# Performance work log

Hardware: AMD Instinct MI355X
Metric: run time of the kernel (lower is better)

## Reference

```python
import jax, jax.numpy as jnp
import numpy as np

D_MODEL = 1024
NUM_HEADS = 16
HEAD_DIM = D_MODEL // NUM_HEADS
SEQ_LEN = 2048
BATCH = 2
THETA = 10000.0


def apply_rope(x, token_positions):
    # x: (..., seq, head_dim); token_positions: (seq,)
    d_k = x.shape[-1]
    inv_freq = 1.0 / (THETA ** (jnp.arange(0, d_k, 2, dtype=jnp.float32) / d_k))  # (d_k/2,)
    angle = token_positions.astype(jnp.float32)[:, None] * inv_freq[None, :]       # (seq, d_k/2)
    cos, sin = jnp.cos(angle), jnp.sin(angle)
    xr = x.reshape(*x.shape[:-1], d_k // 2, 2)
    a, b = xr[..., 0], xr[..., 1]  # real, imag parts of consecutive pairs
    # complex multiply (a + ib) * (cos + i sin)
    out_r = a * cos - b * sin
    out_i = a * sin + b * cos
    return jnp.stack([out_r, out_i], axis=-1).reshape(x.shape)


def setup_inputs() -> dict:
    key = jax.random.key(0)
    ks = jax.random.split(key, 5)
    std = np.sqrt(2.0 / (D_MODEL + D_MODEL))
    return {
        "x": jax.random.normal(ks[0], (BATCH, SEQ_LEN, D_MODEL), dtype=jnp.float32),
        "Wq": jax.random.normal(ks[1], (D_MODEL, D_MODEL), dtype=jnp.float32) * std,
        "Wk": jax.random.normal(ks[2], (D_MODEL, D_MODEL), dtype=jnp.float32) * std,
        "Wv": jax.random.normal(ks[3], (D_MODEL, D_MODEL), dtype=jnp.float32) * std,
        "Wo": jax.random.normal(ks[4], (D_MODEL, D_MODEL), dtype=jnp.float32) * std,
        "token_positions": jnp.arange(SEQ_LEN, dtype=jnp.int32),
    }


def reference(x, Wq, Wk, Wv, Wo, token_positions):
    B, L, D = x.shape
    H, Dh = NUM_HEADS, HEAD_DIM

    def proj(W):  # '... d_in, d_out d_in -> ... d_out' then split heads -> (B,H,L,Dh)
        y = jnp.einsum('bld,ed->ble', x, W)
        return y.reshape(B, L, H, Dh).transpose(0, 2, 1, 3)

    q = apply_rope(proj(Wq), token_positions)
    k = apply_rope(proj(Wk), token_positions)
    v = proj(Wv)

    scores = jnp.einsum('bhqd,bhkd->bhqk', q, k) / jnp.sqrt(jnp.float32(Dh))  # (B,H,L,L)
    causal = jnp.tril(jnp.ones((L, L), dtype=bool))
    scores = jnp.where(causal, scores, -jnp.inf)
    attn = jax.nn.softmax(scores, axis=-1)
    o = jnp.einsum('bhqk,bhkd->bhqd', attn, v)  # (B,H,L,Dh)
    o = o.transpose(0, 2, 1, 3).reshape(B, L, D)
    return jnp.einsum('bld,ed->ble', o, Wo)
```

## Files before the change

kernel.cpp:

```cpp
#include <hip/hip_runtime.h>

typedef __bf16 bf16;
typedef __attribute__((ext_vector_type(8))) __bf16 bf16x8;
typedef __attribute__((ext_vector_type(4))) __bf16 bf16x4;
typedef __attribute__((ext_vector_type(4))) float f32x4;

__device__ inline bf16 f2bf(float f) {
  unsigned u = __builtin_bit_cast(unsigned, f);
  u += 0x7fff + ((u >> 16) & 1);
  unsigned short h = (unsigned short)(u >> 16);
  return __builtin_bit_cast(bf16, h);
}

__device__ inline void gl_lds16(const bf16* g, bf16* l) {
  __builtin_amdgcn_global_load_lds(
      (const __attribute__((address_space(1))) void*)g,
      (__attribute__((address_space(3))) void*)l, 16, 0, 0);
}

__global__ __launch_bounds__(256) void cvt_kernel(
    const float* __restrict__ x, const float* __restrict__ wq,
    const float* __restrict__ wk, const float* __restrict__ wv,
    const float* __restrict__ wo, bf16* __restrict__ dst,
    const int* __restrict__ pos, float* __restrict__ tab) {
  if (blockIdx.x >= 8192) {
    int gid = (blockIdx.x - 8192) * 256 + threadIdx.x;
    int tok = gid >> 5, j = gid & 31;
    float freq = exp2f(-(float)(2 * j) * 0.20762051f);
    float angle = (float)pos[tok] * freq;
    float sn, cs;
    sincosf(angle, &sn, &cs);
    *(float2*)(tab + tok * 64 + j * 2) = make_float2(cs, sn);
    return;
  }
  int idx = (blockIdx.x * 256 + threadIdx.x) * 4;
  const float* src;
  if (idx < 4194304) {
    src = x + idx;
  } else {
    int j = idx - 4194304;
    int w = j >> 20;
    const float* sw = (w == 0) ? wq : (w == 1) ? wk : (w == 2) ? wv : wo;
    src = sw + (j & 1048575);
  }
  float4 f = *(const float4*)src;
  bf16x4 o = {f2bf(f.x), f2bf(f.y), f2bf(f.z), f2bf(f.w)};
  *(bf16x4*)(dst + idx) = o;
}

__global__ __launch_bounds__(256) void gemm_qkv_kernel(
    const bf16* __restrict__ xb, const bf16* __restrict__ wb,
    const float* __restrict__ tab,
    bf16* __restrict__ Qb, bf16* __restrict__ Kb, bf16* __restrict__ Vtb) {
  __shared__ __align__(16) bf16 smem[16384];
  bf16* As = smem;
  bf16* Bs = smem + 8192;
  int tid = threadIdx.x;
  int lane = tid & 63, w = tid >> 6;
  int l15 = lane & 15, quad = lane >> 4;
  int bid = blockIdx.x;
  int xcd = bid & 7, j = bid >> 3;
  int by = (xcd & 3) * 8 + (j & 7);
  int bx = (xcd >> 2) * 12 + (j >> 3);
  int mb = by * 128, nb = bx * 128;
  int mq = (w & 1) * 64, nq = (w >> 1) * 64;
  int gsw = (lane & 7) ^ ((lane >> 3) & 7);
  const bf16* agp = xb + (size_t)(mb + w * 32 + (lane >> 3)) * 1024 + gsw * 8;
  const bf16* bgp = wb + (size_t)(nb + w * 32 + (lane >> 3)) * 1024 + gsw * 8;
  bf16* alp = As + (w * 32) * 64;
  bf16* blp = Bs + (w * 32) * 64;
  f32x4 acc[4][4];
#pragma unroll
  for (int i = 0; i < 4; ++i)
#pragma unroll
    for (int j2 = 0; j2 < 4; ++j2)
      for (int r = 0; r < 4; ++r) acc[i][j2][r] = 0.f;
  for (int kt = 0; kt < 16; ++kt) {
#pragma unroll
    for (int i = 0; i < 4; ++i) {
      gl_lds16(agp + i * 8192, alp + i * 512);
      gl_lds16(bgp + i * 8192, blp + i * 512);
    }
    agp += 64; bgp += 64;
    __syncthreads();
#pragma unroll
    for (int c = 0; c < 2; ++c) {
      bf16x8 af[4], bfr[4];
      int rg = (c * 4 + quad);
#pragma unroll
      for (int mt = 0; mt < 4; ++mt)
        af[mt] = *(const bf16x8*)(As + (mq + mt * 16 + l15) * 64 + (rg ^ (l15 & 7)) * 8);
#pragma unroll
      for (int nt = 0; nt < 4; ++nt)
        bfr[nt] = *(const bf16x8*)(Bs + (nq + nt * 16 + l15) * 64 + (rg ^ (l15 & 7)) * 8);
#pragma unroll
      for (int mt = 0; mt < 4; ++mt)
#pragma unroll
        for (int nt = 0; nt < 4; ++nt)
          acc[mt][nt] = __builtin_amdgcn_mfma_f32_16x16x32_bf16(af[mt], bfr[nt], acc[mt][nt], 0, 0, 0);
    }
    __syncthreads();
  }
  int b = mb >> 11;
  int mtok = mb & 2047;
  if (bx < 16) {
    bf16* dst = (bx < 8) ? Qb : Kb;
#pragma unroll
    for (int nt = 0; nt < 4; ++nt) {
      int e = nb + nq + nt * 16 + l15;
      int d = e & 63;
      int h = (e & 1023) >> 6;
      int tbase = d & ~1;
#pragma unroll
      for (int mt = 0; mt < 4; ++mt) {
#pragma unroll
        for (int r = 0; r < 4; ++r) {
          int ltok = mtok + mq + mt * 16 + quad * 4 + r;
          float val = acc[mt][nt][r];
          float p = __shfl_xor(val, 1);
          float2 cs2 = *(const float2*)(tab + ltok * 64 + tbase);
          float outv = (e & 1) ? (p * cs2.y + val * cs2.x) : (val * cs2.x - p * cs2.y);
          dst[(size_t)(((b << 4) + h) * 2048 + ltok) * 64 + d] = f2bf(outv);
        }
      }
    }
  } else {
    bf16* T = smem;
    for (int h2 = 0; h2 < 2; ++h2) {
      if ((w >> 1) == h2) {
#pragma unroll
        for (int nt = 0; nt < 4; ++nt)
#pragma unroll
          for (int mt = 0; mt < 4; ++mt) {
            bf16x4 tv = {f2bf(acc[mt][nt][0]), f2bf(acc[mt][nt][1]),
                         f2bf(acc[mt][nt][2]), f2bf(acc[mt][nt][3])};
            *(bf16x4*)&T[(nt * 16 + l15) * 136 + mq + mt * 16 + quad * 4] = tv;
          }
      }
      __syncthreads();
      int row = tid >> 2, cs = (tid & 3) * 32;
      int e = nb + h2 * 64 + row;
      int d = e & 63, hh = (e & 1023) >> 6;
      bf16* vdst = Vtb + ((size_t)((b << 4) + hh) * 64 + d) * 2048 + mtok + cs;
#pragma unroll
      for (int j3 = 0; j3 < 4; ++j3)
        *(bf16x8*)(vdst + j3 * 8) = *(const bf16x8*)&T[row * 136 + cs + j3 * 8];
      __syncthreads();
    }
  }
}

#define SCALE_L2E 0.18033688f
__global__ __launch_bounds__(256) void attn_kernel(
    const bf16* __restrict__ Qb, const bf16* __restrict__ Kb,
    const bf16* __restrict__ Vtb, bf16* __restrict__ Ob) {
  __shared__ __align__(16) bf16 Ks[64 * 64];
  __shared__ __align__(16) bf16 Vs[64 * 64];
  __shared__ __align__(16) bf16 pbuf[4][16 * 72];
  int tid = threadIdx.x;
  int lane = tid & 63, w = tid >> 6;
  int l15 = lane & 15, quad = lane >> 4;
  int bidx = blockIdx.x;
  int bh = bidx & 31;
  int qt = 31 - (bidx >> 5);
  int qbase = qt * 64;
  const bf16* Qp = Qb + (size_t)bh * 131072;
  const bf16* Kp = Kb + (size_t)bh * 131072;
  const bf16* Vp = Vtb + (size_t)bh * 131072;
  int r8 = lane >> 3;
  int gsw8 = (lane & 7) ^ r8;
  int g0 = quad ^ (l15 & 7);
  int g1 = (4 + quad) ^ (l15 & 7);
  bf16x8 qf[2];
#pragma unroll
  for (int c = 0; c < 2; ++c)
    qf[c] = *(const bf16x8*)(Qp + (size_t)(qbase + w * 16 + l15) * 64 + c * 32 + quad * 8);
  f32x4 oacc[4];
#pragma unroll
  for (int dt = 0; dt < 4; ++dt)
    for (int r = 0; r < 4; ++r) oacc[dt][r] = 0.f;
  float lpart = 0.f;
  int qmin_w = qbase + w * 16;
  int qmax_w = qmin_w + 15;
  int ntiles = qt + 1;

  for (int t = 0; t < ntiles; ++t) {
    int kb = t * 64;
    {
      const bf16* ksrc = Kp + (size_t)(kb + w * 16 + r8) * 64 + gsw8 * 8;
      bf16* kdst = &Ks[(w * 16) * 64];
      gl_lds16(ksrc, kdst);
      gl_lds16(ksrc + 8 * 64, kdst + 8 * 64);
      const bf16* vsrc = Vp + (size_t)(w * 16 + r8) * 2048 + kb + gsw8 * 8;
      bf16* vdst = &Vs[(w * 16) * 64];
      gl_lds16(vsrc, vdst);
      gl_lds16(vsrc + 8 * 2048, vdst + 8 * 64);
    }
    __syncthreads();
    if (kb <= qmax_w) {
      bf16x8 kf[4][2], vf[4][2];
#pragma unroll
      for (int kt = 0; kt < 4; ++kt) {
        kf[kt][0] = *(const bf16x8*)(&Ks[(kt * 16 + l15) * 64 + g0 * 8]);
        kf[kt][1] = *(const bf16x8*)(&Ks[(kt * 16 + l15) * 64 + g1 * 8]);
      }
#pragma unroll
      for (int dt = 0; dt < 4; ++dt) {
        vf[dt][0] = *(const bf16x8*)(&Vs[(dt * 16 + l15) * 64 + g0 * 8]);
        vf[dt][1] = *(const bf16x8*)(&Vs[(dt * 16 + l15) * 64 + g1 * 8]);
      }
      int q = qmin_w + l15;
      f32x4 s[4];
#pragma unroll
      for (int kt = 0; kt < 4; ++kt) {
        for (int r = 0; r < 4; ++r) s[kt][r] = 0.f;
        s[kt] = __builtin_amdgcn_mfma_f32_16x16x32_bf16(kf[kt][0], qf[0], s[kt], 0, 0, 0);
        s[kt] = __builtin_amdgcn_mfma_f32_16x16x32_bf16(kf[kt][1], qf[1], s[kt], 0, 0, 0);
      }
      float pe[16];
      if (kb + 63 > qmin_w) {
#pragma unroll
        for (int kt = 0; kt < 4; ++kt)
#pragma unroll
          for (int r = 0; r < 4; ++r) {
            int key = kb + kt * 16 + quad * 4 + r;
            pe[kt * 4 + r] = (key <= q) ? exp2f(s[kt][r] * SCALE_L2E) : 0.f;
          }
      } else {
#pragma unroll
        for (int kt = 0; kt < 4; ++kt)
#pragma unroll
          for (int r = 0; r < 4; ++r) pe[kt * 4 + r] = exp2f(s[kt][r] * SCALE_L2E);
      }
#pragma unroll
      for (int i = 0; i < 16; ++i) lpart += pe[i];
#pragma unroll
      for (int kt = 0; kt < 4; ++kt) {
        bf16x4 pw = {f2bf(pe[kt * 4]), f2bf(pe[kt * 4 + 1]), f2bf(pe[kt * 4 + 2]), f2bf(pe[kt * 4 + 3])};
        *(bf16x4*)&pbuf[w][l15 * 72 + kt * 16 + quad * 4] = pw;
      }
      bf16x8 pb0 = *(const bf16x8*)&pbuf[w][l15 * 72 + quad * 8];
      bf16x8 pb1 = *(const bf16x8*)&pbuf[w][l15 * 72 + 32 + quad * 8];
#pragma unroll
      for (int dt = 0; dt < 4; ++dt) {
        oacc[dt] = __builtin_amdgcn_mfma_f32_16x16x32_bf16(vf[dt][0], pb0, oacc[dt], 0, 0, 0);
        oacc[dt] = __builtin_amdgcn_mfma_f32_16x16x32_bf16(vf[dt][1], pb1, oacc[dt], 0, 0, 0);
      }
    }
    __syncthreads();
  }
  float lrun = lpart;
  lrun += __shfl_xor(lrun, 16);
  lrun += __shfl_xor(lrun, 32);
  int b0 = bh >> 4, h = bh & 15;
  float inv = 1.f / lrun;
  int q = qmin_w + l15;
  bf16* obase = Ob + ((size_t)(b0 * 2048 + q)) * 1024 + h * 64;
#pragma unroll
  for (int dt = 0; dt < 4; ++dt)
#pragma unroll
    for (int r = 0; r < 4; ++r)
      obase[dt * 16 + quad * 4 + r] = f2bf(oacc[dt][r] * inv);
}

__global__ __launch_bounds__(256) void gemm_out_kernel(
    const bf16* __restrict__ Ob, const bf16* __restrict__ wob,
    float* __restrict__ out) {
  __shared__ __align__(16) bf16 As[128 * 64];
  __shared__ __align__(16) bf16 Bs[64 * 64];
  int tid = threadIdx.x;
  int lane = tid & 63, w = tid >> 6;
  int l15 = lane & 15, quad = lane >> 4;
  int bid = blockIdx.x;
  int xcd = bid & 7, j = bid >> 3;
  int by = (xcd & 3) * 8 + (j & 7);
  int bx = (xcd >> 2) * 8 + (j >> 3);
  int mb = by * 128, nb = bx * 64;
  int mq = (w & 1) * 64, nq = (w >> 1) * 32;
  int gsw = (lane & 7) ^ ((lane >> 3) & 7);
  const bf16* agp = Ob + (size_t)(mb + w * 32 + (lane >> 3)) * 1024 + gsw * 8;
  const bf16* bgp = wob + (size_t)(nb + w * 16 + (lane >> 3)) * 1024 + gsw * 8;
  bf16* alp = As + (w * 32) * 64;
  bf16* blp = Bs + (w * 16) * 64;
  f32x4 acc[4][2];
#pragma unroll
  for (int i = 0; i < 4; ++i)
#pragma unroll
    for (int j2 = 0; j2 < 2; ++j2)
      for (int r = 0; r < 4; ++r) acc[i][j2][r] = 0.f;
  for (int kt = 0; kt < 16; ++kt) {
#pragma unroll
    for (int i = 0; i < 4; ++i)
      gl_lds16(agp + i * 8192, alp + i * 512);
#pragma unroll
    for (int i = 0; i < 2; ++i)
      gl_lds16(bgp + i * 8192, blp + i * 512);
    agp += 64; bgp += 64;
    __syncthreads();
#pragma unroll
    for (int c = 0; c < 2; ++c) {
      bf16x8 af[4], bfr[2];
      int rg = (c * 4 + quad);
#pragma unroll
      for (int mt = 0; mt < 4; ++mt)
        af[mt] = *(const bf16x8*)(As + (mq + mt * 16 + l15) * 64 + (rg ^ (l15 & 7)) * 8);
#pragma unroll
      for (int nt = 0; nt < 2; ++nt)
        bfr[nt] = *(const bf16x8*)(Bs + (nq + nt * 16 + l15) * 64 + (rg ^ (l15 & 7)) * 8);
#pragma unroll
      for (int mt = 0; mt < 4; ++mt)
#pragma unroll
        for (int nt = 0; nt < 2; ++nt)
          acc[mt][nt] = __builtin_amdgcn_mfma_f32_16x16x32_bf16(af[mt], bfr[nt], acc[mt][nt], 0, 0, 0);
    }
    __syncthreads();
  }
#pragma unroll
  for (int mt = 0; mt < 4; ++mt)
#pragma unroll
    for (int nt = 0; nt < 2; ++nt)
#pragma unroll
      for (int r = 0; r < 4; ++r)
        out[(size_t)(mb + mq + mt * 16 + quad * 4 + r) * 1024 + nb + nq + nt * 16 + l15] = acc[mt][nt][r];
}

extern "C" void kernel_launch(void* const* d_in, const int* in_sizes, int n_in,
                              void* d_out, int out_size, void* d_ws, size_t ws_size,
                              hipStream_t stream) {
  const float* x  = (const float*)d_in[0];
  const float* wq = (const float*)d_in[1];
  const float* wk = (const float*)d_in[2];
  const float* wv = (const float*)d_in[3];
  const float* wo = (const float*)d_in[4];
  const int* pos  = (const int*)d_in[5];
  float* out = (float*)d_out;
  bf16* wsb = (bf16*)d_ws;
  bf16* xb  = wsb;
  bf16* wb  = wsb + 4194304;
  bf16* Qb  = wsb + 8388608;
  bf16* Kb  = wsb + 12582912;
  bf16* Vtb = wsb + 16777216;
  bf16* Obf = wsb + 20971520;
  float* tab = (float*)Obf;
  hipLaunchKernelGGL(cvt_kernel, dim3(8448), dim3(256), 0, stream, x, wq, wk, wv, wo, wsb, pos, tab);
  hipLaunchKernelGGL(gemm_qkv_kernel, dim3(768), dim3(256), 0, stream, xb, wb, tab, Qb, Kb, Vtb);
  hipLaunchKernelGGL(attn_kernel, dim3(1024), dim3(256), 0, stream, Qb, Kb, Vtb, Obf);
  hipLaunchKernelGGL(gemm_out_kernel, dim3(512), dim3(256), 0, stream, Obf, wb + 3 * 1048576, out);
}
```

Measured before the change: 201.7 us.

## Double-buffer QKV GEMM K-loop and prefetch K/V tiles through registers in attention

The QKV GEMM moves from a single 64-wide K tile to double-buffered 32-wide K tiles with a new XOR swizzle, so the global-to-LDS load for the next tile is issued before the MFMAs on the current one. The attention kernel loads the first K/V tile up front, then prefetches the next tile into registers while computing and writes it to LDS after a barrier. It also drops the per-warp causal skip guard. Together this aims to hide global load latency, at the cost of an extra barrier per attention iteration, more registers, and twice as many GEMM loop iterations.

After: 190.2 us. -5.7%, faster.

```diff
diff --git a/kernel.cpp b/kernel.cpp
--- a/kernel.cpp
+++ b/kernel.cpp
@@ -53,8 +53,6 @@
     const float* __restrict__ tab,
     bf16* __restrict__ Qb, bf16* __restrict__ Kb, bf16* __restrict__ Vtb) {
   __shared__ __align__(16) bf16 smem[16384];
-  bf16* As = smem;
-  bf16* Bs = smem + 8192;
   int tid = threadIdx.x;
   int lane = tid & 63, w = tid >> 6;
   int l15 = lane & 15, quad = lane >> 4;
@@ -64,41 +62,49 @@
   int bx = (xcd >> 2) * 12 + (j >> 3);
   int mb = by * 128, nb = bx * 128;
   int mq = (w & 1) * 64, nq = (w >> 1) * 64;
-  int gsw = (lane & 7) ^ ((lane >> 3) & 7);
-  const bf16* agp = xb + (size_t)(mb + w * 32 + (lane >> 3)) * 1024 + gsw * 8;
-  const bf16* bgp = wb + (size_t)(nb + w * 32 + (lane >> 3)) * 1024 + gsw * 8;
-  bf16* alp = As + (w * 32) * 64;
-  bf16* blp = Bs + (w * 32) * 64;
+  int rq = lane >> 2;
+  int gsrc = (lane & 3) ^ (rq & 3) ^ (lane >> 4);
+  const bf16* agp0 = xb + (size_t)(mb + w * 32 + rq) * 1024 + gsrc * 8;
+  const bf16* agp1 = agp0 + 16 * 1024;
+  const bf16* bgp0 = wb + (size_t)(nb + w * 32 + rq) * 1024 + gsrc * 8;
+  const bf16* bgp1 = bgp0 + 16 * 1024;
   f32x4 acc[4][4];
 #pragma unroll
   for (int i = 0; i < 4; ++i)
 #pragma unroll
     for (int j2 = 0; j2 < 4; ++j2)
       for (int r = 0; r < 4; ++r) acc[i][j2][r] = 0.f;
-  for (int kt = 0; kt < 16; ++kt) {
-#pragma unroll
-    for (int i = 0; i < 4; ++i) {
-      gl_lds16(agp + i * 8192, alp + i * 512);
-      gl_lds16(bgp + i * 8192, blp + i * 512);
-    }
-    agp += 64; bgp += 64;
-    __syncthreads();
-#pragma unroll
-    for (int c = 0; c < 2; ++c) {
-      bf16x8 af[4], bfr[4];
-      int rg = (c * 4 + quad);
-#pragma unroll
-      for (int mt = 0; mt < 4; ++mt)
-        af[mt] = *(const bf16x8*)(As + (mq + mt * 16 + l15) * 64 + (rg ^ (l15 & 7)) * 8);
+  gl_lds16(agp0, smem + w * 1024);
+  gl_lds16(agp1, smem + w * 1024 + 512);
+  gl_lds16(bgp0, smem + 4096 + w * 1024);
+  gl_lds16(bgp1, smem + 4096 + w * 1024 + 512);
+  agp0 += 32; agp1 += 32; bgp0 += 32; bgp1 += 32;
+  __syncthreads();
+  int rg = quad ^ (l15 & 3) ^ (l15 >> 2);
+  for (int kt = 0; kt < 32; ++kt) {
+    bf16* Ab = smem + (kt & 1) * 8192;
+    bf16* Bb = Ab + 4096;
+    if (kt < 31) {
+      bf16* An = smem + ((kt & 1) ^ 1) * 8192;
+      bf16* Bn = An + 4096;
+      gl_lds16(agp0, An + w * 1024);
+      gl_lds16(agp1, An + w * 1024 + 512);
+      gl_lds16(bgp0, Bn + w * 1024);
+      gl_lds16(bgp1, Bn + w * 1024 + 512);
+      agp0 += 32; agp1 += 32; bgp0 += 32; bgp1 += 32;
+    }
+    bf16x8 af[4], bfr[4];
+#pragma unroll
+    for (int mt = 0; mt < 4; ++mt)
+      af[mt] = *(const bf16x8*)(Ab + (mq + mt * 16 + l15) * 32 + rg * 8);
+#pragma unroll
+    for (int nt = 0; nt < 4; ++nt)
+      bfr[nt] = *(const bf16x8*)(Bb + (nq + nt * 16 + l15) * 32 + rg * 8);
+#pragma unroll
+    for (int mt = 0; mt < 4; ++mt)
 #pragma unroll
       for (int nt = 0; nt < 4; ++nt)
-        bfr[nt] = *(const bf16x8*)(Bs + (nq + nt * 16 + l15) * 64 + (rg ^ (l15 & 7)) * 8);
-#pragma unroll
-      for (int mt = 0; mt < 4; ++mt)
-#pragma unroll
-        for (int nt = 0; nt < 4; ++nt)
-          acc[mt][nt] = __builtin_amdgcn_mfma_f32_16x16x32_bf16(af[mt], bfr[nt], acc[mt][nt], 0, 0, 0);
-    }
+        acc[mt][nt] = __builtin_amdgcn_mfma_f32_16x16x32_bf16(af[mt], bfr[nt], acc[mt][nt], 0, 0, 0);
     __syncthreads();
   }
   int b = mb >> 11;
@@ -181,23 +187,33 @@
     for (int r = 0; r < 4; ++r) oacc[dt][r] = 0.f;
   float lpart = 0.f;
   int qmin_w = qbase + w * 16;
-  int qmax_w = qmin_w + 15;
   int ntiles = qt + 1;
+
+  {
+    const bf16* ksrc = Kp + (size_t)(w * 16 + r8) * 64 + gsw8 * 8;
+    bf16* kdst = &Ks[(w * 16) * 64];
+    gl_lds16(ksrc, kdst);
+    gl_lds16(ksrc + 8 * 64, kdst + 8 * 64);
+    const bf16* vsrc = Vp + (size_t)(w * 16 + r8) * 2048 + gsw8 * 8;
+    bf16* vdst = &Vs[(w * 16) * 64];
+    gl_lds16(vsrc, vdst);
+    gl_lds16(vsrc + 8 * 2048, vdst + 8 * 64);
+  }
+  __syncthreads();
 
   for (int t = 0; t < ntiles; ++t) {
     int kb = t * 64;
+    bool pf = (t + 1 < ntiles);
+    bf16x8 rk0, rk1, rv0, rv1;
+    if (pf) {
+      const bf16* ksrc = Kp + (size_t)(kb + 64 + w * 16 + r8) * 64 + gsw8 * 8;
+      rk0 = *(const bf16x8*)ksrc;
+      rk1 = *(const bf16x8*)(ksrc + 8 * 64);
+      const bf16* vsrc = Vp + (size_t)(w * 16 + r8) * 2048 + kb + 64 + gsw8 * 8;
+      rv0 = *(const bf16x8*)vsrc;
+      rv1 = *(const bf16x8*)(vsrc + 8 * 2048);
+    }
     {
-      const bf16* ksrc = Kp + (size_t)(kb + w * 16 + r8) * 64 + gsw8 * 8;
-      bf16* kdst = &Ks[(w * 16) * 64];
-      gl_lds16(ksrc, kdst);
-      gl_lds16(ksrc + 8 * 64, kdst + 8 * 64);
-      const bf16* vsrc = Vp + (size_t)(w * 16 + r8) * 2048 + kb + gsw8 * 8;
-      bf16* vdst = &Vs[(w * 16) * 64];
-      gl_lds16(vsrc, vdst);
-      gl_lds16(vsrc + 8 * 2048, vdst + 8 * 64);
-    }
-    __syncthreads();
-    if (kb <= qmax_w) {
       bf16x8 kf[4][2], vf[4][2];
 #pragma unroll
       for (int kt = 0; kt < 4; ++kt) {
@@ -246,6 +262,15 @@
         oacc[dt] = __builtin_amdgcn_mfma_f32_16x16x32_bf16(vf[dt][0], pb0, oacc[dt], 0, 0, 0);
         oacc[dt] = __builtin_amdgcn_mfma_f32_16x16x32_bf16(vf[dt][1], pb1, oacc[dt], 0, 0, 0);
       }
+    }
+    __syncthreads();
+    if (pf) {
+      bf16* kd = &Ks[(w * 16) * 64] + lane * 8;
+      *(bf16x8*)kd = rk0;
+      *(bf16x8*)(kd + 512) = rk1;
+      bf16* vd = &Vs[(w * 16) * 64] + lane * 8;
+      *(bf16x8*)vd = rv0;
+      *(bf16x8*)(vd + 512) = rv1;
     }
     __syncthreads();
   }
```
